# Kernel optimization log

Hardware: AMD Instinct MI355X
Metric: run time of the kernel (lower is better)

Reference implementation:

```python
import jax, jax.numpy as jnp
import numpy as np

INPUT_DIM, HIDDEN, LATENT, HEADS = 4, 32, 2, 4
N_NODES, N_EDGES = 50000, 800000
EPS_BN = 1e-5
NEG_SLOPE = 0.2


def _glorot(key, shape):
    fan_in, fan_out = shape[0], shape[-1]
    lim = jnp.sqrt(6.0 / (fan_in + fan_out))
    return jax.random.uniform(key, shape, jnp.float32, -lim, lim)


def setup_inputs() -> dict:
    key = jax.random.key(0)
    ks = jax.random.split(key, 20)
    x = jax.random.normal(ks[0], (N_NODES, INPUT_DIM), jnp.float32)
    edge_index = jax.random.randint(ks[1], (2, N_EDGES), 0, N_NODES, jnp.int64)

    def gat_params(k, in_ch, out_ch, heads, concat):
        k1, k2, k3 = jax.random.split(k, 3)
        W = _glorot(k1, (in_ch, heads * out_ch))
        a_src = _glorot(k2, (heads, out_ch))
        a_dst = _glorot(k3, (heads, out_ch))
        b = jnp.zeros((heads * out_ch,) if concat else (out_ch,), jnp.float32)
        return W, a_src, a_dst, b

    w_e1, as_e1, ad_e1, b_e1 = gat_params(ks[2], INPUT_DIM, HIDDEN, HEADS, True)
    w_e3, as_e3, ad_e3, b_e3 = gat_params(ks[3], HIDDEN * HEADS, LATENT, 1, False)
    w_d1, as_d1, ad_d1, b_d1 = gat_params(ks[4], LATENT, HIDDEN, HEADS, True)
    w_d3, as_d3, ad_d3, b_d3 = gat_params(ks[5], HIDDEN * HEADS, INPUT_DIM, 1, False)

    return dict(
        x=x, edge_index=edge_index,
        bn_gamma=jnp.ones((INPUT_DIM,), jnp.float32),
        bn_beta=jnp.zeros((INPUT_DIM,), jnp.float32),
        w_e1=w_e1, as_e1=as_e1, ad_e1=ad_e1, b_e1=b_e1,
        w_e3=w_e3, as_e3=as_e3, ad_e3=ad_e3, b_e3=b_e3,
        w_d1=w_d1, as_d1=as_d1, ad_d1=ad_d1, b_d1=b_d1,
        w_d3=w_d3, as_d3=as_d3, ad_d3=ad_d3, b_d3=b_d3,
    )


def gat_conv(x, src, dst, W, a_src, a_dst, b, heads, out_ch, concat):
    """PyG-style GATConv: gather -> attention -> segment softmax -> scatter."""
    n = x.shape[0]
    h = (x @ W).reshape(n, heads, out_ch)                 # [N,H,C]
    alpha_s = jnp.sum(h * a_src, axis=-1)                 # [N,H]
    alpha_d = jnp.sum(h * a_dst, axis=-1)                 # [N,H]
    e = jax.nn.leaky_relu(alpha_s[src] + alpha_d[dst], NEG_SLOPE)  # [E,H]
    # numerically-stable softmax over incoming edges of each dst node
    m = jax.ops.segment_max(e, dst, num_segments=n)
    e = jnp.exp(e - m[dst])
    s = jax.ops.segment_sum(e, dst, num_segments=n)
    a = e / (s[dst] + 1e-16)                              # [E,H]
    msg = h[src] * a[:, :, None]                          # [E,H,C]
    out = jax.ops.segment_sum(msg, dst, num_segments=n)   # [N,H,C]
    out = out.reshape(n, heads * out_ch) if concat else out.mean(axis=1)
    return out + b


def reference(x, edge_index, bn_gamma, bn_beta,
              w_e1, as_e1, ad_e1, b_e1,
              w_e3, as_e3, ad_e3, b_e3,
              w_d1, as_d1, ad_d1, b_d1,
              w_d3, as_d3, ad_d3, b_d3):
    n = x.shape[0]
    # GATConv default add_self_loops=True
    loops = jnp.arange(n, dtype=edge_index.dtype)
    src = jnp.concatenate([edge_index[0], loops])
    dst = jnp.concatenate([edge_index[1], loops])

    # BatchNorm1d (training-mode batch statistics, biased variance)
    mu = x.mean(axis=0)
    var = x.var(axis=0)
    x_in = (x - mu) * jax.lax.rsqrt(var + EPS_BN) * bn_gamma + bn_beta

    enc1 = jax.nn.relu(gat_conv(x_in, src, dst, w_e1, as_e1, ad_e1, b_e1, HEADS, HIDDEN, True))
    latent = gat_conv(enc1, src, dst, w_e3, as_e3, ad_e3, b_e3, 1, LATENT, False)
    dec1 = jax.nn.relu(gat_conv(latent, src, dst, w_d1, as_d1, ad_d1, b_d1, HEADS, HIDDEN, True))
    x_out = gat_conv(dec1, src, dst, w_d3, as_d3, ad_d3, b_d3, 1, INPUT_DIM, False)
    return x_out
```

## Files before the change

### kernel.cpp

```cpp
#include <hip/hip_runtime.h>

#define NN 50000
#define E0 800000
#define ET 850000
#define EPS_BN 1e-5f
#define SLOPE 0.2f
#define NBP 32
#define EPC 2048
#define NCH 416
#define PBITS 10
#define NP 49
#define SCN (NP*NCH)

__device__ __forceinline__ float lrelu(float v){ return v > 0.f ? v : SLOPE*v; }

__global__ __launch_bounds__(256) void chunk_hist_bn(const int* __restrict__ ei, int* __restrict__ chunkcnt,
                                                     const float* __restrict__ x, float* __restrict__ part){
  __shared__ int cc[NP];
  for (int i=threadIdx.x; i<NP; i+=256) cc[i]=0;
  __syncthreads();
  int base = blockIdx.x*EPC;
  int end = min(base+EPC, ET);
  for (int e = base+threadIdx.x; e < end; e += 256){
    int dst = (e < E0) ? ei[E0 + e] : (e - E0);
    atomicAdd(&cc[dst>>PBITS], 1);
  }
  __syncthreads();
  for (int i=threadIdx.x; i<NP; i+=256) chunkcnt[blockIdx.x*NP + i] = cc[i];

  if (blockIdx.x < NBP){
    float s[4]={0,0,0,0}, q[4]={0,0,0,0};
    for (int n = blockIdx.x*256 + threadIdx.x; n < NN; n += NBP*256){
      float4 v = reinterpret_cast<const float4*>(x)[n];
      s[0]+=v.x; s[1]+=v.y; s[2]+=v.z; s[3]+=v.w;
      q[0]+=v.x*v.x; q[1]+=v.y*v.y; q[2]+=v.z*v.z; q[3]+=v.w*v.w;
    }
    #pragma unroll
    for (int m=1;m<64;m<<=1){
      #pragma unroll
      for (int i=0;i<4;i++){ s[i]+=__shfl_xor(s[i],m); q[i]+=__shfl_xor(q[i],m); }
    }
    __shared__ float lds[4][8];
    int wid = threadIdx.x>>6, lane = threadIdx.x&63;
    if (lane==0){
      #pragma unroll
      for (int i=0;i<4;i++){ lds[wid][i]=s[i]; lds[wid][4+i]=q[i]; }
    }
    __syncthreads();
    if (threadIdx.x < 8){
      float p = lds[0][threadIdx.x]+lds[1][threadIdx.x]+lds[2][threadIdx.x]+lds[3][threadIdx.x];
      part[blockIdx.x*8 + threadIdx.x] = p;
    }
  }
}

__global__ __launch_bounds__(1024) void scan_fold(
    const int* __restrict__ chunkcnt, int* __restrict__ pofs,
    const float* __restrict__ part, const float* __restrict__ gamma, const float* __restrict__ beta,
    const float* __restrict__ w_e1, const float* __restrict__ as_e1, const float* __restrict__ ad_e1,
    const float* __restrict__ w_d1, const float* __restrict__ as_d1, const float* __restrict__ ad_d1,
    float* __restrict__ sclsft, float* __restrict__ fold){
  __shared__ int wsum[1024];
  int t = threadIdx.x;
  const int PER = (SCN + 1023)/1024;
  int vals[PER];
  int mysum = 0;
  #pragma unroll
  for (int k=0;k<PER;k++){
    int idx = t*PER + k;
    int v = 0;
    if (idx < SCN){ int p = idx/NCH, ch = idx - p*NCH; v = chunkcnt[ch*NP + p]; }
    vals[k] = v; mysum += v;
  }
  wsum[t] = mysum; __syncthreads();
  int val = mysum;
  for (int off=1; off<1024; off<<=1){
    int tmp = (t>=off) ? wsum[t-off] : 0;
    __syncthreads();
    val += tmp; wsum[t] = val; __syncthreads();
  }
  int run = val - mysum;
  #pragma unroll
  for (int k=0;k<PER;k++){
    int idx = t*PER + k;
    if (idx < SCN){ int p = idx/NCH, ch = idx - p*NCH; pofs[ch*NP + p] = run; }
    run += vals[k];
  }

  if (t < 64){
    int ch = t&7, bslot = t>>3;
    float s = 0.f;
    for (int b=bslot; b<NBP; b+=8) s += part[b*8 + ch];
    s += __shfl_xor(s,8); s += __shfl_xor(s,16); s += __shfl_xor(s,32);
    float qv = __shfl(s, (t&3)+4);
    if (t < 4){
      float mu  = s*(1.0f/NN);
      float var = qv*(1.0f/NN) - mu*mu;
      float scl = rsqrtf(var + EPS_BN)*gamma[t];
      sclsft[t]   = scl;
      sclsft[4+t] = beta[t] - mu*scl;
    }
  } else if (t < 128){
    int u = t - 64;
    if (u < 32){
      int idx = u & 15; int h = idx>>2; int i = idx&3;
      const float* a = (u<16) ? as_e1 : ad_e1;
      float sum = 0.f;
      for (int c=0;c<32;c++) sum += w_e1[i*128 + h*32 + c] * a[h*32 + c];
      fold[u] = sum;
    } else if (u < 48){
      int idx = u - 32; int j = idx & 7; int h = j>>1; int i = j&1;
      const float* a = (idx<8) ? as_d1 : ad_d1;
      float sum = 0.f;
      for (int c=0;c<32;c++) sum += w_d1[i*128 + h*32 + c] * a[h*32 + c];
      fold[32 + idx] = sum;
    }
  }
}

__global__ __launch_bounds__(256) void partition_pass(const int* __restrict__ ei,
                                                      const int* __restrict__ pofs,
                                                      int2* __restrict__ pedge){
  __shared__ int cur[NP];
  for (int i=threadIdx.x; i<NP; i+=256) cur[i] = pofs[blockIdx.x*NP + i];
  __syncthreads();
  int base = blockIdx.x*EPC;
  int end = min(base+EPC, ET);
  for (int e = base+threadIdx.x; e < end; e += 256){
    int src, dst;
    if (e < E0){ src = ei[e]; dst = ei[E0+e]; } else { src = dst = e - E0; }
    int pos = atomicAdd(&cur[dst>>PBITS], 1);
    pedge[pos] = make_int2(src, dst);
  }
}

__global__ __launch_bounds__(1024) void fine_build(const int2* __restrict__ pedge,
                                                   const int* __restrict__ pofs,
                                                   int* __restrict__ rowptr, int* __restrict__ ssrc){
  int p = blockIdx.x;
  int pstart = pofs[p];
  int pend = (p+1 < NP) ? pofs[p+1] : ET;
  int dbase = p << PBITS;
  __shared__ int hist[1<<PBITS];
  __shared__ int cur[1<<PBITS];
  int t = threadIdx.x;
  hist[t] = 0;
  __syncthreads();
  for (int i = pstart + t; i < pend; i += 1024)
    atomicAdd(&hist[pedge[i].y - dbase], 1);
  __syncthreads();
  int orig = hist[t];
  __syncthreads();
  int v = orig;
  for (int off=1; off<1024; off<<=1){
    int tmp = (t>=off) ? hist[t-off] : 0;
    __syncthreads();
    v += tmp; hist[t] = v; __syncthreads();
  }
  int excl = v - orig;
  int d = dbase + t;
  if (d < NN) rowptr[d] = pstart + excl;
  if (p == NP-1 && t == 0) rowptr[NN] = ET;
  cur[t] = pstart + excl;
  __syncthreads();
  for (int i = pstart + t; i < pend; i += 1024){
    int2 e = pedge[i];
    int pos = atomicAdd(&cur[e.y - dbase], 1);
    ssrc[pos] = e.x;
  }
}

__global__ __launch_bounds__(256) void node1(
    const float* __restrict__ x, const float* __restrict__ sclsft, const float* __restrict__ fold,
    float* __restrict__ pk1, float* __restrict__ ald1){
  int n = blockIdx.x*256 + threadIdx.x;
  if (n >= NN) return;
  float4 v = reinterpret_cast<const float4*>(x)[n];
  float xb[4] = {v.x, v.y, v.z, v.w};
  #pragma unroll
  for (int i=0;i<4;i++) xb[i] = xb[i]*sclsft[i] + sclsft[4+i];
  float4 s4, d4;
  float* sp = &s4.x; float* dp = &d4.x;
  #pragma unroll
  for (int h=0;h<4;h++){
    float s=0.f, d=0.f;
    #pragma unroll
    for (int i=0;i<4;i++){ s += xb[i]*fold[h*4+i]; d += xb[i]*fold[16+h*4+i]; }
    sp[h]=s; dp[h]=d;
  }
  reinterpret_cast<float4*>(pk1)[n*2+0] = s4;
  reinterpret_cast<float4*>(pk1)[n*2+1] = make_float4(xb[0],xb[1],xb[2],xb[3]);
  reinterpret_cast<float4*>(ald1)[n] = d4;
}

template<int NC>
__global__ __launch_bounds__(256) void eagg_h4(
    const float* __restrict__ pk, const float* __restrict__ ald,
    const int* __restrict__ rowptr, const int* __restrict__ ssrc,
    float* __restrict__ out){
  int dst = blockIdx.x*32 + (threadIdx.x>>3);
  int sub = threadIdx.x & 7;
  if (dst >= NN) return;
  int eslot = sub>>2, head = sub&3;
  int r0 = rowptr[dst], r1 = rowptr[dst+1];
  float adv = ald[(size_t)dst*4 + head];
  float sum = 0.f, acc[NC];
  #pragma unroll
  for (int c=0;c<NC;c++) acc[c]=0.f;
  for (int i=r0+eslot; i<r1; i+=2){
    int s = ssrc[i];
    const float* base = pk + (size_t)s*8;
    float w = __expf(lrelu(base[head] + adv));
    sum += w;
    if constexpr (NC==4){
      float4 f = *reinterpret_cast<const float4*>(base+4);
      acc[0]+=w*f.x; acc[1]+=w*f.y; acc[2]+=w*f.z; acc[3]+=w*f.w;
    } else {
      float2 f = *reinterpret_cast<const float2*>(base+4);
      acc[0]+=w*f.x; acc[1]+=w*f.y;
    }
  }
  sum += __shfl_xor(sum, 4);
  #pragma unroll
  for (int c=0;c<NC;c++) acc[c] += __shfl_xor(acc[c], 4);
  if (eslot==0){
    float inv = 1.f/(sum+1e-16f);
    if constexpr (NC==4){
      reinterpret_cast<float4*>(out)[(size_t)dst*4 + head] =
        make_float4(acc[0]*inv, acc[1]*inv, acc[2]*inv, acc[3]*inv);
    } else {
      reinterpret_cast<float2*>(out)[(size_t)dst*4 + head] =
        make_float2(acc[0]*inv, acc[1]*inv);
    }
  }
}

template<int NC, int STRIDE, int AOFF, int FOFF, int EPI>
__global__ __launch_bounds__(256) void eagg_h1(
    const float* __restrict__ pk, const float* __restrict__ ald,
    const int* __restrict__ rowptr, const int* __restrict__ ssrc,
    const float* __restrict__ bias, const float* __restrict__ fold,
    float* __restrict__ out, float* __restrict__ ald_out){
  int dst = blockIdx.x*32 + (threadIdx.x>>3);
  int sub = threadIdx.x & 7;
  if (dst >= NN) return;
  int r0 = rowptr[dst], r1 = rowptr[dst+1];
  float adv = ald[dst];
  float sum = 0.f, acc[NC];
  #pragma unroll
  for (int c=0;c<NC;c++) acc[c]=0.f;
  for (int i=r0+sub; i<r1; i+=8){
    int s = ssrc[i];
    const float* base = pk + (size_t)s*STRIDE;
    float w = __expf(lrelu(base[AOFF] + adv));
    sum += w;
    if constexpr (NC==2){
      float2 f = *reinterpret_cast<const float2*>(base+FOFF);
      acc[0]+=w*f.x; acc[1]+=w*f.y;
    } else {
      float4 f = *reinterpret_cast<const float4*>(base+FOFF);
      acc[0]+=w*f.x; acc[1]+=w*f.y; acc[2]+=w*f.z; acc[3]+=w*f.w;
    }
  }
  #pragma unroll
  for (int m=1;m<8;m<<=1){
    sum += __shfl_xor(sum,m);
    #pragma unroll
    for (int c=0;c<NC;c++) acc[c] += __shfl_xor(acc[c],m);
  }
  if (sub != 0) return;
  float inv = 1.f/(sum+1e-16f);
  if constexpr (EPI==2){
    float l0 = acc[0]*inv + bias[0];
    float l1 = acc[1]*inv + bias[1];
    float4 s3, d3; float* sp=&s3.x; float* dp=&d3.x;
    #pragma unroll
    for (int h=0;h<4;h++){
      sp[h] = l0*fold[32+h*2+0] + l1*fold[32+h*2+1];
      dp[h] = l0*fold[40+h*2+0] + l1*fold[40+h*2+1];
    }
    reinterpret_cast<float4*>(out)[(size_t)dst*2] = s3;
    out[(size_t)dst*8+4] = l0;
    out[(size_t)dst*8+5] = l1;
    reinterpret_cast<float4*>(ald_out)[dst] = d3;
  } else {
    reinterpret_cast<float4*>(out)[dst] =
      make_float4(acc[0]*inv+bias[0], acc[1]*inv+bias[1],
                  acc[2]*inv+bias[2], acc[3]*inv+bias[3]);
  }
}

__global__ __launch_bounds__(256) void post1(
    const float* __restrict__ agg1, const float* __restrict__ w_e1, const float* __restrict__ b_e1,
    const float* __restrict__ w_e3, const float* __restrict__ as_e3, const float* __restrict__ ad_e3,
    float* __restrict__ pk2, float* __restrict__ ald2){
  int lane = threadIdx.x & 63;
  int n = blockIdx.x*4 + (threadIdx.x>>6);
  int oc0 = lane, oc1 = lane + 64;
  int h0 = oc0>>5, h1 = oc1>>5;
  float4 a0 = reinterpret_cast<const float4*>(agg1)[n*4 + h0];
  float4 a1 = reinterpret_cast<const float4*>(agg1)[n*4 + h1];
  float e0 = b_e1[oc0] + a0.x*w_e1[0*128+oc0] + a0.y*w_e1[1*128+oc0]
                       + a0.z*w_e1[2*128+oc0] + a0.w*w_e1[3*128+oc0];
  float e1 = b_e1[oc1] + a1.x*w_e1[0*128+oc1] + a1.y*w_e1[1*128+oc1]
                       + a1.z*w_e1[2*128+oc1] + a1.w*w_e1[3*128+oc1];
  e0 = fmaxf(e0, 0.f); e1 = fmaxf(e1, 0.f);
  float p0 = e0*w_e3[oc0*2+0] + e1*w_e3[oc1*2+0];
  float p1 = e0*w_e3[oc0*2+1] + e1*w_e3[oc1*2+1];
  #pragma unroll
  for (int m=1;m<64;m<<=1){ p0 += __shfl_xor(p0,m); p1 += __shfl_xor(p1,m); }
  if (lane==0){
    reinterpret_cast<float4*>(pk2)[n] =
      make_float4(p0, p1, p0*as_e3[0]+p1*as_e3[1], 0.f);
    ald2[n] = p0*ad_e3[0] + p1*ad_e3[1];
  }
}

__global__ __launch_bounds__(256) void post3(
    const float* __restrict__ agg3, const float* __restrict__ w_d1, const float* __restrict__ b_d1,
    const float* __restrict__ w_d3, const float* __restrict__ as_d3, const float* __restrict__ ad_d3,
    float* __restrict__ pk4, float* __restrict__ ald4){
  int lane = threadIdx.x & 63;
  int n = blockIdx.x*4 + (threadIdx.x>>6);
  int oc0 = lane, oc1 = lane + 64;
  int h0 = oc0>>5, h1 = oc1>>5;
  float2 a0 = reinterpret_cast<const float2*>(agg3)[n*4 + h0];
  float2 a1 = reinterpret_cast<const float2*>(agg3)[n*4 + h1];
  float e0 = b_d1[oc0] + a0.x*w_d1[0*128+oc0] + a0.y*w_d1[1*128+oc0];
  float e1 = b_d1[oc1] + a1.x*w_d1[0*128+oc1] + a1.y*w_d1[1*128+oc1];
  e0 = fmaxf(e0, 0.f); e1 = fmaxf(e1, 0.f);
  float p[4];
  #pragma unroll
  for (int c=0;c<4;c++) p[c] = e0*w_d3[oc0*4+c] + e1*w_d3[oc1*4+c];
  #pragma unroll
  for (int m=1;m<64;m<<=1){
    #pragma unroll
    for (int c=0;c<4;c++) p[c] += __shfl_xor(p[c],m);
  }
  if (lane==0){
    float s=0.f, d=0.f;
    #pragma unroll
    for (int c=0;c<4;c++){ s += p[c]*as_d3[c]; d += p[c]*ad_d3[c]; }
    pk4[(size_t)n*8] = s;
    reinterpret_cast<float4*>(pk4 + (size_t)n*8 + 4)[0] = make_float4(p[0],p[1],p[2],p[3]);
    ald4[n] = d;
  }
}

extern "C" void kernel_launch(void* const* d_in, const int* in_sizes, int n_in,
                              void* d_out, int out_size, void* d_ws, size_t ws_size,
                              hipStream_t stream) {
  const float* x     = (const float*)d_in[0];
  const int*   ei    = (const int*)  d_in[1];
  const float* gamma = (const float*)d_in[2];
  const float* beta  = (const float*)d_in[3];
  const float* w_e1  = (const float*)d_in[4];
  const float* as_e1 = (const float*)d_in[5];
  const float* ad_e1 = (const float*)d_in[6];
  const float* b_e1  = (const float*)d_in[7];
  const float* w_e3  = (const float*)d_in[8];
  const float* as_e3 = (const float*)d_in[9];
  const float* ad_e3 = (const float*)d_in[10];
  const float* b_e3  = (const float*)d_in[11];
  const float* w_d1  = (const float*)d_in[12];
  const float* as_d1 = (const float*)d_in[13];
  const float* ad_d1 = (const float*)d_in[14];
  const float* b_d1  = (const float*)d_in[15];
  const float* w_d3  = (const float*)d_in[16];
  const float* as_d3 = (const float*)d_in[17];
  const float* ad_d3 = (const float*)d_in[18];
  const float* b_d3  = (const float*)d_in[19];

  char* ws = (char*)d_ws;
  size_t off = 0;
  auto alloc = [&](size_t bytes)->void*{
    void* p = ws + off;
    off += (bytes + 255) & ~(size_t)255;
    return p;
  };
  int*   chunkcnt = (int*)  alloc((size_t)NCH*NP*4);
  int*   pofs     = (int*)  alloc((size_t)NCH*NP*4);
  int2*  pedge    = (int2*) alloc((size_t)ET*8);
  int*   rowptr   = (int*)  alloc((size_t)(NN+1)*4);
  int*   ssrc     = (int*)  alloc((size_t)ET*4);
  float* part     = (float*)alloc((size_t)NBP*8*4);
  float* sclsft   = (float*)alloc(32);
  float* fold     = (float*)alloc(64*4);
  float* pk1      = (float*)alloc((size_t)NN*8*4);
  float* ald1     = (float*)alloc((size_t)NN*4*4);
  float* agg1     = (float*)alloc((size_t)NN*16*4);
  float* pk2      = (float*)alloc((size_t)NN*4*4);
  float* ald2     = (float*)alloc((size_t)NN*4);
  float* pk3      = (float*)alloc((size_t)NN*8*4);
  float* ald3     = (float*)alloc((size_t)NN*4*4);
  float* agg3     = (float*)alloc((size_t)NN*8*4);
  float* pk4      = (float*)alloc((size_t)NN*8*4);
  float* ald4     = (float*)alloc((size_t)NN*4);

  chunk_hist_bn<<<NCH, 256, 0, stream>>>(ei, chunkcnt, x, part);
  scan_fold<<<1, 1024, 0, stream>>>(chunkcnt, pofs, part, gamma, beta,
                                    w_e1, as_e1, ad_e1, w_d1, as_d1, ad_d1, sclsft, fold);
  partition_pass<<<NCH, 256, 0, stream>>>(ei, pofs, pedge);
  fine_build<<<NP, 1024, 0, stream>>>(pedge, pofs, rowptr, ssrc);

  const int AGG_BLOCKS = (NN+31)/32;

  node1<<<(NN+255)/256, 256, 0, stream>>>(x, sclsft, fold, pk1, ald1);
  eagg_h4<4><<<AGG_BLOCKS, 256, 0, stream>>>(pk1, ald1, rowptr, ssrc, agg1);
  post1<<<NN/4, 256, 0, stream>>>(agg1, w_e1, b_e1, w_e3, as_e3, ad_e3, pk2, ald2);
  eagg_h1<2,4,2,0,2><<<AGG_BLOCKS, 256, 0, stream>>>(pk2, ald2, rowptr, ssrc, b_e3, fold, pk3, ald3);
  eagg_h4<2><<<AGG_BLOCKS, 256, 0, stream>>>(pk3, ald3, rowptr, ssrc, agg3);
  post3<<<NN/4, 256, 0, stream>>>(agg3, w_d1, b_d1, w_d3, as_d3, ad_d3, pk4, ald4);
  eagg_h1<4,8,0,4,4><<<AGG_BLOCKS, 256, 0, stream>>>(pk4, ald4, rowptr, ssrc, b_d3, nullptr, (float*)d_out, nullptr);
}
```

Measured before the change: 126.4 us.

## Fuse post-aggregation dense layers into GAT edge-aggregation kernels

Merges post1 into the first aggregation kernel and post3 into the third. Each 8-lane group now handles all four heads for its destination over 8 edge slots, then computes the 128-wide hidden projection and the next layer's projection in-register using shuffles. This removes two kernel launches and the agg1/agg3 intermediate round trips through global memory. The last layer's gather is split into separate feat4 and s4a arrays. In exchange, per-edge register and ALU work per lane grows, and every lane reloads the weight vectors.

```diff
diff --git a/kernel.cpp b/kernel.cpp
--- a/kernel.cpp
+++ b/kernel.cpp
@@ -193,158 +193,215 @@
   reinterpret_cast<float4*>(ald1)[n] = d4;
 }
 
-template<int NC>
-__global__ __launch_bounds__(256) void eagg_h4(
-    const float* __restrict__ pk, const float* __restrict__ ald,
+__global__ __launch_bounds__(256) void eagg1(
+    const float* __restrict__ pk1, const float* __restrict__ ald,
     const int* __restrict__ rowptr, const int* __restrict__ ssrc,
-    float* __restrict__ out){
-  int dst = blockIdx.x*32 + (threadIdx.x>>3);
-  int sub = threadIdx.x & 7;
-  if (dst >= NN) return;
-  int eslot = sub>>2, head = sub&3;
-  int r0 = rowptr[dst], r1 = rowptr[dst+1];
-  float adv = ald[(size_t)dst*4 + head];
-  float sum = 0.f, acc[NC];
-  #pragma unroll
-  for (int c=0;c<NC;c++) acc[c]=0.f;
-  for (int i=r0+eslot; i<r1; i+=2){
-    int s = ssrc[i];
-    const float* base = pk + (size_t)s*8;
-    float w = __expf(lrelu(base[head] + adv));
-    sum += w;
-    if constexpr (NC==4){
-      float4 f = *reinterpret_cast<const float4*>(base+4);
-      acc[0]+=w*f.x; acc[1]+=w*f.y; acc[2]+=w*f.z; acc[3]+=w*f.w;
-    } else {
-      float2 f = *reinterpret_cast<const float2*>(base+4);
-      acc[0]+=w*f.x; acc[1]+=w*f.y;
-    }
-  }
-  sum += __shfl_xor(sum, 4);
-  #pragma unroll
-  for (int c=0;c<NC;c++) acc[c] += __shfl_xor(acc[c], 4);
-  if (eslot==0){
-    float inv = 1.f/(sum+1e-16f);
-    if constexpr (NC==4){
-      reinterpret_cast<float4*>(out)[(size_t)dst*4 + head] =
-        make_float4(acc[0]*inv, acc[1]*inv, acc[2]*inv, acc[3]*inv);
-    } else {
-      reinterpret_cast<float2*>(out)[(size_t)dst*4 + head] =
-        make_float2(acc[0]*inv, acc[1]*inv);
-    }
-  }
-}
-
-template<int NC, int STRIDE, int AOFF, int FOFF, int EPI>
-__global__ __launch_bounds__(256) void eagg_h1(
-    const float* __restrict__ pk, const float* __restrict__ ald,
-    const int* __restrict__ rowptr, const int* __restrict__ ssrc,
-    const float* __restrict__ bias, const float* __restrict__ fold,
-    float* __restrict__ out, float* __restrict__ ald_out){
+    const float* __restrict__ w_e1, const float* __restrict__ b_e1,
+    const float* __restrict__ w_e3, const float* __restrict__ as_e3, const float* __restrict__ ad_e3,
+    float* __restrict__ pk2, float* __restrict__ ald2){
   int dst = blockIdx.x*32 + (threadIdx.x>>3);
   int sub = threadIdx.x & 7;
   if (dst >= NN) return;
   int r0 = rowptr[dst], r1 = rowptr[dst+1];
-  float adv = ald[dst];
-  float sum = 0.f, acc[NC];
-  #pragma unroll
-  for (int c=0;c<NC;c++) acc[c]=0.f;
-  for (int i=r0+sub; i<r1; i+=8){
+  float4 advv = reinterpret_cast<const float4*>(ald)[dst];
+  float adv[4] = {advv.x, advv.y, advv.z, advv.w};
+  float sum[4] = {0,0,0,0};
+  float acc[4][4] = {{0,0,0,0},{0,0,0,0},{0,0,0,0},{0,0,0,0}};
+  for (int i = r0 + sub; i < r1; i += 8){
     int s = ssrc[i];
-    const float* base = pk + (size_t)s*STRIDE;
-    float w = __expf(lrelu(base[AOFF] + adv));
-    sum += w;
-    if constexpr (NC==2){
-      float2 f = *reinterpret_cast<const float2*>(base+FOFF);
-      acc[0]+=w*f.x; acc[1]+=w*f.y;
-    } else {
-      float4 f = *reinterpret_cast<const float4*>(base+FOFF);
-      acc[0]+=w*f.x; acc[1]+=w*f.y; acc[2]+=w*f.z; acc[3]+=w*f.w;
-    }
+    float4 a = reinterpret_cast<const float4*>(pk1)[s*2+0];
+    float4 f = reinterpret_cast<const float4*>(pk1)[s*2+1];
+    float av[4] = {a.x,a.y,a.z,a.w};
+    #pragma unroll
+    for (int h=0;h<4;h++){
+      float w = __expf(lrelu(av[h]+adv[h]));
+      sum[h] += w;
+      acc[h][0] += w*f.x; acc[h][1] += w*f.y; acc[h][2] += w*f.z; acc[h][3] += w*f.w;
+    }
+  }
+  #pragma unroll
+  for (int m=1;m<8;m<<=1){
+    #pragma unroll
+    for (int h=0;h<4;h++){
+      sum[h] += __shfl_xor(sum[h],m);
+      #pragma unroll
+      for (int c=0;c<4;c++) acc[h][c] += __shfl_xor(acc[h][c],m);
+    }
+  }
+  int hh = sub>>1;
+  float G0=acc[0][0], G1=acc[0][1], G2=acc[0][2], G3=acc[0][3], GS=sum[0];
+  #pragma unroll
+  for (int h=1;h<4;h++){
+    if (hh==h){ G0=acc[h][0]; G1=acc[h][1]; G2=acc[h][2]; G3=acc[h][3]; GS=sum[h]; }
+  }
+  float ginv = 1.f/(GS+1e-16f);
+  G0*=ginv; G1*=ginv; G2*=ginv; G3*=ginv;
+  float p0 = 0.f, p1 = 0.f;
+  int ocb = sub*16;
+  #pragma unroll
+  for (int q=0;q<4;q++){
+    int o = ocb + q*4;
+    float4 b  = *reinterpret_cast<const float4*>(b_e1 + o);
+    float4 w0 = *reinterpret_cast<const float4*>(w_e1 + 0*128 + o);
+    float4 w1 = *reinterpret_cast<const float4*>(w_e1 + 1*128 + o);
+    float4 w2 = *reinterpret_cast<const float4*>(w_e1 + 2*128 + o);
+    float4 w3 = *reinterpret_cast<const float4*>(w_e1 + 3*128 + o);
+    float e0 = fmaxf(b.x + G0*w0.x + G1*w1.x + G2*w2.x + G3*w3.x, 0.f);
+    float e1 = fmaxf(b.y + G0*w0.y + G1*w1.y + G2*w2.y + G3*w3.y, 0.f);
+    float e2 = fmaxf(b.z + G0*w0.z + G1*w1.z + G2*w2.z + G3*w3.z, 0.f);
+    float e3 = fmaxf(b.w + G0*w0.w + G1*w1.w + G2*w2.w + G3*w3.w, 0.f);
+    float4 wa = *reinterpret_cast<const float4*>(w_e3 + o*2);
+    float4 wb = *reinterpret_cast<const float4*>(w_e3 + o*2 + 4);
+    p0 += e0*wa.x + e1*wa.z + e2*wb.x + e3*wb.z;
+    p1 += e0*wa.y + e1*wa.w + e2*wb.y + e3*wb.w;
+  }
+  #pragma unroll
+  for (int m=1;m<8;m<<=1){ p0 += __shfl_xor(p0,m); p1 += __shfl_xor(p1,m); }
+  if (sub==0){
+    reinterpret_cast<float4*>(pk2)[dst] = make_float4(p0, p1, p0*as_e3[0]+p1*as_e3[1], 0.f);
+    ald2[dst] = p0*ad_e3[0] + p1*ad_e3[1];
+  }
+}
+
+__global__ __launch_bounds__(256) void eagg2(
+    const float* __restrict__ pk2, const float* __restrict__ ald2,
+    const int* __restrict__ rowptr, const int* __restrict__ ssrc,
+    const float* __restrict__ b_e3, const float* __restrict__ fold,
+    float* __restrict__ pk3, float* __restrict__ ald3){
+  int dst = blockIdx.x*32 + (threadIdx.x>>3);
+  int sub = threadIdx.x & 7;
+  if (dst >= NN) return;
+  int r0 = rowptr[dst], r1 = rowptr[dst+1];
+  float adv = ald2[dst];
+  float sum = 0.f, a0 = 0.f, a1 = 0.f;
+  for (int i = r0 + sub; i < r1; i += 8){
+    int s = ssrc[i];
+    float4 r = reinterpret_cast<const float4*>(pk2)[s];
+    float w = __expf(lrelu(r.z + adv));
+    sum += w; a0 += w*r.x; a1 += w*r.y;
+  }
+  #pragma unroll
+  for (int m=1;m<8;m<<=1){
+    sum += __shfl_xor(sum,m); a0 += __shfl_xor(a0,m); a1 += __shfl_xor(a1,m);
+  }
+  if (sub != 0) return;
+  float inv = 1.f/(sum+1e-16f);
+  float l0 = a0*inv + b_e3[0];
+  float l1 = a1*inv + b_e3[1];
+  float4 s3, d3; float* sp=&s3.x; float* dp=&d3.x;
+  #pragma unroll
+  for (int h=0;h<4;h++){
+    sp[h] = l0*fold[32+h*2+0] + l1*fold[32+h*2+1];
+    dp[h] = l0*fold[40+h*2+0] + l1*fold[40+h*2+1];
+  }
+  reinterpret_cast<float4*>(pk3)[dst*2] = s3;
+  pk3[(size_t)dst*8+4] = l0;
+  pk3[(size_t)dst*8+5] = l1;
+  reinterpret_cast<float4*>(ald3)[dst] = d3;
+}
+
+__global__ __launch_bounds__(256) void eagg3(
+    const float* __restrict__ pk3, const float* __restrict__ ald3,
+    const int* __restrict__ rowptr, const int* __restrict__ ssrc,
+    const float* __restrict__ w_d1, const float* __restrict__ b_d1,
+    const float* __restrict__ w_d3, const float* __restrict__ as_d3, const float* __restrict__ ad_d3,
+    float4* __restrict__ feat4, float* __restrict__ s4a, float* __restrict__ ald4){
+  int dst = blockIdx.x*32 + (threadIdx.x>>3);
+  int sub = threadIdx.x & 7;
+  if (dst >= NN) return;
+  int r0 = rowptr[dst], r1 = rowptr[dst+1];
+  float4 advv = reinterpret_cast<const float4*>(ald3)[dst];
+  float adv[4] = {advv.x, advv.y, advv.z, advv.w};
+  float sum[4] = {0,0,0,0};
+  float acc[4][2] = {{0,0},{0,0},{0,0},{0,0}};
+  for (int i = r0 + sub; i < r1; i += 8){
+    int s = ssrc[i];
+    float4 a = reinterpret_cast<const float4*>(pk3)[s*2+0];
+    float2 f = *reinterpret_cast<const float2*>(pk3 + (size_t)s*8 + 4);
+    float av[4] = {a.x,a.y,a.z,a.w};
+    #pragma unroll
+    for (int h=0;h<4;h++){
+      float w = __expf(lrelu(av[h]+adv[h]));
+      sum[h] += w;
+      acc[h][0] += w*f.x; acc[h][1] += w*f.y;
+    }
+  }
+  #pragma unroll
+  for (int m=1;m<8;m<<=1){
+    #pragma unroll
+    for (int h=0;h<4;h++){
+      sum[h] += __shfl_xor(sum[h],m);
+      acc[h][0] += __shfl_xor(acc[h][0],m);
+      acc[h][1] += __shfl_xor(acc[h][1],m);
+    }
+  }
+  int hh = sub>>1;
+  float G0=acc[0][0], G1=acc[0][1], GS=sum[0];
+  #pragma unroll
+  for (int h=1;h<4;h++){
+    if (hh==h){ G0=acc[h][0]; G1=acc[h][1]; GS=sum[h]; }
+  }
+  float ginv = 1.f/(GS+1e-16f);
+  G0*=ginv; G1*=ginv;
+  float p0=0.f,p1=0.f,p2=0.f,p3=0.f;
+  int ocb = sub*16;
+  #pragma unroll
+  for (int q=0;q<4;q++){
+    int o = ocb + q*4;
+    float4 b  = *reinterpret_cast<const float4*>(b_d1 + o);
+    float4 w0 = *reinterpret_cast<const float4*>(w_d1 + 0*128 + o);
+    float4 w1 = *reinterpret_cast<const float4*>(w_d1 + 1*128 + o);
+    float e0 = fmaxf(b.x + G0*w0.x + G1*w1.x, 0.f);
+    float e1 = fmaxf(b.y + G0*w0.y + G1*w1.y, 0.f);
+    float e2 = fmaxf(b.z + G0*w0.z + G1*w1.z, 0.f);
+    float e3 = fmaxf(b.w + G0*w0.w + G1*w1.w, 0.f);
+    float4 d0 = *reinterpret_cast<const float4*>(w_d3 + (o+0)*4);
+    float4 d1 = *reinterpret_cast<const float4*>(w_d3 + (o+1)*4);
+    float4 d2 = *reinterpret_cast<const float4*>(w_d3 + (o+2)*4);
+    float4 d3v = *reinterpret_cast<const float4*>(w_d3 + (o+3)*4);
+    p0 += e0*d0.x + e1*d1.x + e2*d2.x + e3*d3v.x;
+    p1 += e0*d0.y + e1*d1.y + e2*d2.y + e3*d3v.y;
+    p2 += e0*d0.z + e1*d1.z + e2*d2.z + e3*d3v.z;
+    p3 += e0*d0.w + e1*d1.w + e2*d2.w + e3*d3v.w;
+  }
+  #pragma unroll
+  for (int m=1;m<8;m<<=1){
+    p0 += __shfl_xor(p0,m); p1 += __shfl_xor(p1,m);
+    p2 += __shfl_xor(p2,m); p3 += __shfl_xor(p3,m);
+  }
+  if (sub==0){
+    feat4[dst] = make_float4(p0,p1,p2,p3);
+    s4a[dst]  = p0*as_d3[0]+p1*as_d3[1]+p2*as_d3[2]+p3*as_d3[3];
+    ald4[dst] = p0*ad_d3[0]+p1*ad_d3[1]+p2*ad_d3[2]+p3*ad_d3[3];
+  }
+}
+
+__global__ __launch_bounds__(256) void eagg4(
+    const float4* __restrict__ feat4, const float* __restrict__ s4a, const float* __restrict__ ald4,
+    const int* __restrict__ rowptr, const int* __restrict__ ssrc,
+    const float* __restrict__ b_d3, float* __restrict__ out){
+  int dst = blockIdx.x*32 + (threadIdx.x>>3);
+  int sub = threadIdx.x & 7;
+  if (dst >= NN) return;
+  int r0 = rowptr[dst], r1 = rowptr[dst+1];
+  float adv = ald4[dst];
+  float sum = 0.f, a0=0.f, a1=0.f, a2=0.f, a3=0.f;
+  for (int i = r0 + sub; i < r1; i += 8){
+    int s = ssrc[i];
+    float w = __expf(lrelu(s4a[s] + adv));
+    float4 f = feat4[s];
+    sum += w; a0 += w*f.x; a1 += w*f.y; a2 += w*f.z; a3 += w*f.w;
   }
   #pragma unroll
   for (int m=1;m<8;m<<=1){
     sum += __shfl_xor(sum,m);
-    #pragma unroll
-    for (int c=0;c<NC;c++) acc[c] += __shfl_xor(acc[c],m);
+    a0 += __shfl_xor(a0,m); a1 += __shfl_xor(a1,m);
+    a2 += __shfl_xor(a2,m); a3 += __shfl_xor(a3,m);
   }
   if (sub != 0) return;
   float inv = 1.f/(sum+1e-16f);
-  if constexpr (EPI==2){
-    float l0 = acc[0]*inv + bias[0];
-    float l1 = acc[1]*inv + bias[1];
-    float4 s3, d3; float* sp=&s3.x; float* dp=&d3.x;
-    #pragma unroll
-    for (int h=0;h<4;h++){
-      sp[h] = l0*fold[32+h*2+0] + l1*fold[32+h*2+1];
-      dp[h] = l0*fold[40+h*2+0] + l1*fold[40+h*2+1];
-    }
-    reinterpret_cast<float4*>(out)[(size_t)dst*2] = s3;
-    out[(size_t)dst*8+4] = l0;
-    out[(size_t)dst*8+5] = l1;
-    reinterpret_cast<float4*>(ald_out)[dst] = d3;
-  } else {
-    reinterpret_cast<float4*>(out)[dst] =
-      make_float4(acc[0]*inv+bias[0], acc[1]*inv+bias[1],
-                  acc[2]*inv+bias[2], acc[3]*inv+bias[3]);
-  }
-}
-
-__global__ __launch_bounds__(256) void post1(
-    const float* __restrict__ agg1, const float* __restrict__ w_e1, const float* __restrict__ b_e1,
-    const float* __restrict__ w_e3, const float* __restrict__ as_e3, const float* __restrict__ ad_e3,
-    float* __restrict__ pk2, float* __restrict__ ald2){
-  int lane = threadIdx.x & 63;
-  int n = blockIdx.x*4 + (threadIdx.x>>6);
-  int oc0 = lane, oc1 = lane + 64;
-  int h0 = oc0>>5, h1 = oc1>>5;
-  float4 a0 = reinterpret_cast<const float4*>(agg1)[n*4 + h0];
-  float4 a1 = reinterpret_cast<const float4*>(agg1)[n*4 + h1];
-  float e0 = b_e1[oc0] + a0.x*w_e1[0*128+oc0] + a0.y*w_e1[1*128+oc0]
-                       + a0.z*w_e1[2*128+oc0] + a0.w*w_e1[3*128+oc0];
-  float e1 = b_e1[oc1] + a1.x*w_e1[0*128+oc1] + a1.y*w_e1[1*128+oc1]
-                       + a1.z*w_e1[2*128+oc1] + a1.w*w_e1[3*128+oc1];
-  e0 = fmaxf(e0, 0.f); e1 = fmaxf(e1, 0.f);
-  float p0 = e0*w_e3[oc0*2+0] + e1*w_e3[oc1*2+0];
-  float p1 = e0*w_e3[oc0*2+1] + e1*w_e3[oc1*2+1];
-  #pragma unroll
-  for (int m=1;m<64;m<<=1){ p0 += __shfl_xor(p0,m); p1 += __shfl_xor(p1,m); }
-  if (lane==0){
-    reinterpret_cast<float4*>(pk2)[n] =
-      make_float4(p0, p1, p0*as_e3[0]+p1*as_e3[1], 0.f);
-    ald2[n] = p0*ad_e3[0] + p1*ad_e3[1];
-  }
-}
-
-__global__ __launch_bounds__(256) void post3(
-    const float* __restrict__ agg3, const float* __restrict__ w_d1, const float* __restrict__ b_d1,
-    const float* __restrict__ w_d3, const float* __restrict__ as_d3, const float* __restrict__ ad_d3,
-    float* __restrict__ pk4, float* __restrict__ ald4){
-  int lane = threadIdx.x & 63;
-  int n = blockIdx.x*4 + (threadIdx.x>>6);
-  int oc0 = lane, oc1 = lane + 64;
-  int h0 = oc0>>5, h1 = oc1>>5;
-  float2 a0 = reinterpret_cast<const float2*>(agg3)[n*4 + h0];
-  float2 a1 = reinterpret_cast<const float2*>(agg3)[n*4 + h1];
-  float e0 = b_d1[oc0] + a0.x*w_d1[0*128+oc0] + a0.y*w_d1[1*128+oc0];
-  float e1 = b_d1[oc1] + a1.x*w_d1[0*128+oc1] + a1.y*w_d1[1*128+oc1];
-  e0 = fmaxf(e0, 0.f); e1 = fmaxf(e1, 0.f);
-  float p[4];
-  #pragma unroll
-  for (int c=0;c<4;c++) p[c] = e0*w_d3[oc0*4+c] + e1*w_d3[oc1*4+c];
-  #pragma unroll
-  for (int m=1;m<64;m<<=1){
-    #pragma unroll
-    for (int c=0;c<4;c++) p[c] += __shfl_xor(p[c],m);
-  }
-  if (lane==0){
-    float s=0.f, d=0.f;
-    #pragma unroll
-    for (int c=0;c<4;c++){ s += p[c]*as_d3[c]; d += p[c]*ad_d3[c]; }
-    pk4[(size_t)n*8] = s;
-    reinterpret_cast<float4*>(pk4 + (size_t)n*8 + 4)[0] = make_float4(p[0],p[1],p[2],p[3]);
-    ald4[n] = d;
-  }
+  reinterpret_cast<float4*>(out)[dst] =
+    make_float4(a0*inv+b_d3[0], a1*inv+b_d3[1], a2*inv+b_d3[2], a3*inv+b_d3[3]);
 }
 
 extern "C" void kernel_launch(void* const* d_in, const int* in_sizes, int n_in,
@@ -388,13 +445,12 @@
   float* fold     = (float*)alloc(64*4);
   float* pk1      = (float*)alloc((size_t)NN*8*4);
   float* ald1     = (float*)alloc((size_t)NN*4*4);
-  float* agg1     = (float*)alloc((size_t)NN*16*4);
   float* pk2      = (float*)alloc((size_t)NN*4*4);
   float* ald2     = (float*)alloc((size_t)NN*4);
   float* pk3      = (float*)alloc((size_t)NN*8*4);
   float* ald3     = (float*)alloc((size_t)NN*4*4);
-  float* agg3     = (float*)alloc((size_t)NN*8*4);
-  float* pk4      = (float*)alloc((size_t)NN*8*4);
+  float4* feat4   = (float4*)alloc((size_t)NN*4*4);
+  float* s4a      = (float*)alloc((size_t)NN*4);
   float* ald4     = (float*)alloc((size_t)NN*4);
 
   chunk_hist_bn<<<NCH, 256, 0, stream>>>(ei, chunkcnt, x, part);
@@ -406,10 +462,10 @@
   const int AGG_BLOCKS = (NN+31)/32;
 
   node1<<<(NN+255)/256, 256, 0, stream>>>(x, sclsft, fold, pk1, ald1);
-  eagg_h4<4><<<AGG_BLOCKS, 256, 0, stream>>>(pk1, ald1, rowptr, ssrc, agg1);
-  post1<<<NN/4, 256, 0, stream>>>(agg1, w_e1, b_e1, w_e3, as_e3, ad_e3, pk2, ald2);
-  eagg_h1<2,4,2,0,2><<<AGG_BLOCKS, 256, 0, stream>>>(pk2, ald2, rowptr, ssrc, b_e3, fold, pk3, ald3);
-  eagg_h4<2><<<AGG_BLOCKS, 256, 0, stream>>>(pk3, ald3, rowptr, ssrc, agg3);
-  post3<<<NN/4, 256, 0, stream>>>(agg3, w_d1, b_d1, w_d3, as_d3, ad_d3, pk4, ald4);
-  eagg_h1<4,8,0,4,4><<<AGG_BLOCKS, 256, 0, stream>>>(pk4, ald4, rowptr, ssrc, b_d3, nullptr, (float*)d_out, nullptr);
-}
+  eagg1<<<AGG_BLOCKS, 256, 0, stream>>>(pk1, ald1, rowptr, ssrc,
+                                        w_e1, b_e1, w_e3, as_e3, ad_e3, pk2, ald2);
+  eagg2<<<AGG_BLOCKS, 256, 0, stream>>>(pk2, ald2, rowptr, ssrc, b_e3, fold, pk3, ald3);
+  eagg3<<<AGG_BLOCKS, 256, 0, stream>>>(pk3, ald3, rowptr, ssrc,
+                                        w_d1, b_d1, w_d3, as_d3, ad_d3, feat4, s4a, ald4);
+  eagg4<<<AGG_BLOCKS, 256, 0, stream>>>(feat4, s4a, ald4, rowptr, ssrc, b_d3, (float*)d_out);
+}
```

After: 127.9 us. Within noise of the previous version (+1.2%).
